# Kernel optimization log

Hardware: AMD Instinct MI355X
Metric: run time of the kernel (lower is better)

## Reference

```python
import jax, jax.numpy as jnp
import numpy as np

B, T, E, A, D, S, N, K = 256, 64, 1024, 32, 1024, 256, 1024, 5
MIN_STD = 0.1


def setup_inputs() -> dict:
    key = jax.random.key(0)
    ks = jax.random.split(key, 16)
    def w(k, shape, scale=0.02):
        return jax.random.normal(k, shape, jnp.float32) * scale
    return dict(
        seq_len=T,
        obs_embed=jax.random.normal(ks[0], (B, T, E), jnp.float32),
        action=jax.random.normal(ks[1], (B, T, A), jnp.float32),
        nonterms=jnp.ones((B, T, 1), jnp.float32),
        init_deter=jax.random.normal(ks[2], (B, D), jnp.float32),
        init_stoch=jax.random.normal(ks[3], (B, S), jnp.float32),
        noise_prior=jax.random.normal(ks[4], (T - 1, B, S), jnp.float32),
        noise_post=jax.random.normal(ks[5], (T - 1, B, S), jnp.float32),
        W_embed=w(ks[6], (S + A, D)), b_embed=jnp.zeros((D,), jnp.float32),
        W_ens=w(ks[7], (K, D, S)), b_ens=jnp.zeros((K, S), jnp.float32),
        W_ih=w(ks[8], (3 * D, D)), W_hh=w(ks[9], (3 * D, D)),
        b_ih=jnp.zeros((3 * D,), jnp.float32), b_hh=jnp.zeros((3 * D,), jnp.float32),
        Wp1=w(ks[10], (D, N)), bp1=jnp.zeros((N,), jnp.float32),
        Wp2=w(ks[11], (N, 2 * S)), bp2=jnp.zeros((2 * S,), jnp.float32),
        Wq1=w(ks[12], (D + E, N)), bq1=jnp.zeros((N,), jnp.float32),
        Wq2=w(ks[13], (N, 2 * S)), bq2=jnp.zeros((2 * S,), jnp.float32),
    )


def _rollout(obs_embed, action, nonterms, init_deter, init_stoch,
             noise_prior, noise_post, W_embed, b_embed, W_ens, b_ens,
             W_ih, W_hh, b_ih, b_hh, Wp1, bp1, Wp2, bp2, Wq1, bq1, Wq2, bq2):
    elu = jax.nn.elu

    def gru(x, h):  # torch.nn.GRUCell math
        gi = x @ W_ih.T + b_ih
        gh = h @ W_hh.T + b_hh
        ir, iz, ig = jnp.split(gi, 3, axis=-1)
        hr, hz, hg = jnp.split(gh, 3, axis=-1)
        r = jax.nn.sigmoid(ir + hr)
        z = jax.nn.sigmoid(iz + hz)
        n = jnp.tanh(ig + r * hg)
        return (1.0 - z) * n + z * h

    def step(carry, xs):
        deter, stoch = carry
        obs_t, act_t, nt, eps_p, eps_q = xs  # nt: [B,1]
        prev_action = act_t * nt
        sa = elu(jnp.concatenate([stoch * nt, prev_action], -1) @ W_embed + b_embed)
        preds = jnp.einsum('bd,kds->kbs', sa, W_ens) + b_ens[:, None, :]  # ensemble heads
        deter_new = gru(sa, deter * nt)
        pm, ps = jnp.split(elu(deter_new @ Wp1 + bp1) @ Wp2 + bp2, 2, -1)
        ps = jax.nn.softplus(ps) + MIN_STD
        prior_stoch = pm + ps * eps_p
        qm, qs = jnp.split(elu(jnp.concatenate([deter_new, obs_t], -1) @ Wq1 + bq1) @ Wq2 + bq2, 2, -1)
        qs = jax.nn.softplus(qs) + MIN_STD
        post_stoch = qm + qs * eps_q
        prior_cat = jnp.concatenate([pm, ps, prior_stoch, deter_new], -1)   # [B, 3S+D]
        post_cat = jnp.concatenate([qm, qs, post_stoch, deter_new], -1)     # [B, 3S+D]
        disag_flat = jnp.transpose(preds, (1, 0, 2)).reshape(preds.shape[1], -1)  # [B, K*S]
        out = jnp.concatenate([prior_cat, post_cat, disag_flat], -1)
        return (deter_new, post_stoch), out

    Tm1 = noise_prior.shape[0]
    xs = (jnp.swapaxes(obs_embed[:, :Tm1], 0, 1),
          jnp.swapaxes(action[:, :Tm1], 0, 1),
          jnp.swapaxes(nonterms[:, :Tm1], 0, 1),
          noise_prior, noise_post)
    _, outs = jax.lax.scan(step, (init_deter, init_stoch), xs)
    return jnp.swapaxes(outs, 0, 1)  # [B, T-1, 2*(3S+D)+K*S]


def reference(seq_len, obs_embed, action, nonterms, init_deter, init_stoch,
              noise_prior, noise_post, W_embed, b_embed, W_ens, b_ens,
              W_ih, W_hh, b_ih, b_hh, Wp1, bp1, Wp2, bp2, Wq1, bq1, Wq2, bq2):
    return _rollout(obs_embed, action, nonterms, init_deter, init_stoch,
                    noise_prior, noise_post, W_embed, b_embed, W_ens, b_ens,
                    W_ih, W_hh, b_ih, b_hh, Wp1, bp1, Wp2, bp2, Wq1, bq1, Wq2, bq2)
```

## Files before the change

kernel.cpp:

```cpp
#include <hip/hip_runtime.h>

typedef float f32x4 __attribute__((ext_vector_type(4)));
typedef __bf16 bf16x8 __attribute__((ext_vector_type(8)));
typedef unsigned short u16;

#define NB 256
#define TT 64
#define TM1 63
#define DD 1024
#define SS 256
#define EE 1024
#define AD 32
#define OUTC 4864
#define OUTT ((size_t)TM1 * OUTC)

__device__ __forceinline__ u16 f2bf(float f) {
    unsigned u = __float_as_uint(f);
    u += 0x7FFFu + ((u >> 16) & 1u);
    return (u16)(u >> 16);
}
__device__ __forceinline__ float sigm(float x) { return 1.f / (1.f + expf(-x)); }
__device__ __forceinline__ float splus(float x) { return x > 15.f ? x : log1pf(expf(x)); }
__device__ __forceinline__ float eluf(float x) { return x > 0.f ? x : (expf(x) - 1.f); }
__device__ __forceinline__ int swz(int row, int cb) { return row * 128 + (cb ^ ((row & 7) << 4)); }

template <class FA, class FE>
__device__ __forceinline__ void gemm_tile(char* As, char* Bs, FA fa,
                                          const u16* __restrict__ Bt, int ldb,
                                          int K, int m0, int n0, FE fe) {
    const int tid = threadIdx.x;
    const int lane = tid & 63;
    const int w = tid >> 6;
    const int wr = (w >> 1) * 32, wc = (w & 1) * 32;
    f32x4 acc00 = {}, acc01 = {}, acc10 = {}, acc11 = {};
    const int r0 = tid >> 3;
    const int ke = (tid & 7) * 8;
    const int cb = (tid & 7) * 16;

    for (int k0 = 0; k0 < K; k0 += 64) {
        uint4 av0 = fa(m0 + r0, k0 + ke);
        uint4 av1 = fa(m0 + r0 + 32, k0 + ke);
        uint4 bv0 = *(const uint4*)(Bt + (size_t)(n0 + r0) * ldb + k0 + ke);
        uint4 bv1 = *(const uint4*)(Bt + (size_t)(n0 + r0 + 32) * ldb + k0 + ke);
        __syncthreads();
        *(uint4*)(As + swz(r0, cb)) = av0;
        *(uint4*)(As + swz(r0 + 32, cb)) = av1;
        *(uint4*)(Bs + swz(r0, cb)) = bv0;
        *(uint4*)(Bs + swz(r0 + 32, cb)) = bv1;
        __syncthreads();
#pragma unroll
        for (int kk = 0; kk < 64; kk += 32) {
            const int fcb = kk * 2 + (lane >> 4) * 16;
            bf16x8 a0 = *(const bf16x8*)(As + swz(wr + (lane & 15), fcb));
            bf16x8 a1 = *(const bf16x8*)(As + swz(wr + 16 + (lane & 15), fcb));
            bf16x8 b0 = *(const bf16x8*)(Bs + swz(wc + (lane & 15), fcb));
            bf16x8 b1 = *(const bf16x8*)(Bs + swz(wc + 16 + (lane & 15), fcb));
            acc00 = __builtin_amdgcn_mfma_f32_16x16x32_bf16(a0, b0, acc00, 0, 0, 0);
            acc01 = __builtin_amdgcn_mfma_f32_16x16x32_bf16(a0, b1, acc01, 0, 0, 0);
            acc10 = __builtin_amdgcn_mfma_f32_16x16x32_bf16(a1, b0, acc10, 0, 0, 0);
            acc11 = __builtin_amdgcn_mfma_f32_16x16x32_bf16(a1, b1, acc11, 0, 0, 0);
        }
    }
    const int er = (lane >> 4) * 4, ec = lane & 15;
#pragma unroll
    for (int r = 0; r < 4; r++) {
        fe(m0 + wr + er + r, n0 + wc + ec, acc00[r]);
        fe(m0 + wr + er + r, n0 + wc + 16 + ec, acc01[r]);
        fe(m0 + wr + 16 + er + r, n0 + wc + ec, acc10[r]);
        fe(m0 + wr + 16 + er + r, n0 + wc + 16 + ec, acc11[r]);
    }
}

__global__ void __launch_bounds__(256) k_cast(const float* __restrict__ in,
                                              u16* __restrict__ out, int n) {
    int i = blockIdx.x * 256 + threadIdx.x;
    if (i < n) out[i] = f2bf(in[i]);
}

__global__ void __launch_bounds__(256) k_transpose(const float* __restrict__ in,
                                                   u16* __restrict__ out,
                                                   int R, int C, int Rpad, int total) {
    int i = blockIdx.x * 256 + threadIdx.x;
    if (i >= total) return;
    int r = i % Rpad;
    int bc = i / Rpad;
    int c = bc % C;
    int bb = bc / C;
    out[i] = (r < R) ? f2bf(in[((size_t)bb * R + r) * C + c]) : (u16)0;
}

__global__ void __launch_bounds__(256) k_prep0(const float* __restrict__ init_deter,
                                               const float* __restrict__ init_stoch,
                                               const float* __restrict__ action,
                                               const float* __restrict__ nonterms,
                                               float* __restrict__ deter,
                                               u16* __restrict__ h_nt,
                                               u16* __restrict__ x_embed) {
    int idx = blockIdx.x * 256 + threadIdx.x;
    int b = idx >> 10, d = idx & 1023;
    float nt0 = nonterms[b * TT + 0];
    float dv = init_deter[idx];
    deter[idx] = dv;
    h_nt[idx] = f2bf(dv * nt0);
    if (d < 256) {
        x_embed[b * 320 + d] = f2bf(init_stoch[b * 256 + d] * nt0);
    } else if (d < 320) {
        int c = d - 256;
        x_embed[b * 320 + d] = (c < AD) ? f2bf(action[(size_t)b * TT * AD + c] * nt0) : (u16)0;
    }
}

__global__ void __launch_bounds__(256) k_gru(const float* __restrict__ gi,
                                             const float* __restrict__ gh,
                                             float* __restrict__ deter,
                                             const float* __restrict__ nonterms, int t,
                                             u16* __restrict__ deter_b,
                                             float* __restrict__ out) {
    int idx = blockIdx.x * 256 + threadIdx.x;
    int b = idx >> 10, d = idx & 1023;
    float nt = nonterms[b * TT + t];
    float h = deter[idx] * nt;
    size_t gb = (size_t)b * 3072;
    float r = sigm(gi[gb + d] + gh[gb + d]);
    float z = sigm(gi[gb + 1024 + d] + gh[gb + 1024 + d]);
    float n = tanhf(gi[gb + 2048 + d] + r * gh[gb + 2048 + d]);
    float dn = (1.f - z) * n + z * h;
    deter[idx] = dn;
    deter_b[idx] = f2bf(dn);
    float* ob = out + (size_t)b * OUTT + (size_t)t * OUTC;
    ob[768 + d] = dn;
    ob[2560 + d] = dn;
}

__global__ void __launch_bounds__(256) k_dist(const float* __restrict__ pout,
                                              const float* __restrict__ qout,
                                              const float* __restrict__ noise_p,
                                              const float* __restrict__ noise_q, int t,
                                              const float* __restrict__ deter,
                                              const float* __restrict__ action,
                                              const float* __restrict__ nonterms,
                                              float* __restrict__ out,
                                              u16* __restrict__ x_embed,
                                              u16* __restrict__ h_nt) {
    int idx = blockIdx.x * 256 + threadIdx.x;
    int b = idx >> 10, d = idx & 1023;
    float ntn = nonterms[b * TT + (t + 1)];
    h_nt[idx] = f2bf(deter[idx] * ntn);
    float* ob = out + (size_t)b * OUTT + (size_t)t * OUTC;
    if (d < 256) {
        int s = d;
        float pm = pout[b * 512 + s];
        float ps = splus(pout[b * 512 + 256 + s]) + 0.1f;
        float ep = noise_p[(size_t)t * (NB * SS) + b * SS + s];
        float pst = pm + ps * ep;
        ob[s] = pm;
        ob[256 + s] = ps;
        ob[512 + s] = pst;
        float qm = qout[b * 512 + s];
        float qs = splus(qout[b * 512 + 256 + s]) + 0.1f;
        float eq = noise_q[(size_t)t * (NB * SS) + b * SS + s];
        float qst = qm + qs * eq;
        ob[1792 + s] = qm;
        ob[2048 + s] = qs;
        ob[2304 + s] = qst;
        x_embed[b * 320 + s] = f2bf(qst * ntn);
    } else if (d < 320) {
        int c = d - 256;
        u16 v = 0;
        if (c < AD) v = f2bf(action[(size_t)b * TT * AD + (size_t)(t + 1) * AD + c] * ntn);
        x_embed[b * 320 + 256 + c] = v;
    }
}

__global__ void __launch_bounds__(256) k_gemm_sa(const u16* __restrict__ xe,
                                                 const u16* __restrict__ Wt,
                                                 const float* __restrict__ bias,
                                                 u16* __restrict__ sa) {
    __shared__ char As[8192];
    __shared__ char Bs[8192];
    int m0 = blockIdx.y * 64, n0 = blockIdx.x * 64;
    auto fa = [&](int r, int k) { return *(const uint4*)(xe + r * 320 + k); };
    auto fe = [&](int r, int n, float v) {
        v = eluf(v + bias[n]);
        sa[r * 1024 + n] = f2bf(v);
    };
    gemm_tile(As, Bs, fa, Wt, 320, 320, m0, n0, fe);
}

__global__ void __launch_bounds__(256) k_gemm_big(const u16* __restrict__ sa,
                                                  const u16* __restrict__ hnt,
                                                  const u16* __restrict__ Wih,
                                                  const u16* __restrict__ Whh,
                                                  const u16* __restrict__ Wens,
                                                  const float* __restrict__ bih,
                                                  const float* __restrict__ bhh,
                                                  const float* __restrict__ bens,
                                                  float* __restrict__ gi,
                                                  float* __restrict__ gh,
                                                  float* __restrict__ dout, int t) {
    __shared__ char As[8192];
    __shared__ char Bs[8192];
    int z = blockIdx.z;
    int m0 = blockIdx.y * 64, n0 = blockIdx.x * 64;
    if (z == 2 && n0 >= 1280) return;
    const u16* Ap = (z == 1) ? hnt : sa;
    auto fa = [&](int r, int k) { return *(const uint4*)(Ap + r * 1024 + k); };
    if (z == 0) {
        auto fe = [&](int r, int n, float v) { gi[(size_t)r * 3072 + n] = v + bih[n]; };
        gemm_tile(As, Bs, fa, Wih, 1024, 1024, m0, n0, fe);
    } else if (z == 1) {
        auto fe = [&](int r, int n, float v) { gh[(size_t)r * 3072 + n] = v + bhh[n]; };
        gemm_tile(As, Bs, fa, Whh, 1024, 1024, m0, n0, fe);
    } else {
        float* op = dout + (size_t)t * OUTC + 3584;
        auto fe = [&](int r, int n, float v) { op[(size_t)r * OUTT + n] = v + bens[n]; };
        gemm_tile(As, Bs, fa, Wens, 1024, 1024, m0, n0, fe);
    }
}

__global__ void __launch_bounds__(256) k_gemm_hpq(const u16* __restrict__ dtb,
                                                  const float* __restrict__ obs,
                                                  const u16* __restrict__ Wp1t,
                                                  const u16* __restrict__ Wq1t,
                                                  const float* __restrict__ bp1,
                                                  const float* __restrict__ bq1,
                                                  u16* __restrict__ hp,
                                                  u16* __restrict__ hq, int t) {
    __shared__ char As[8192];
    __shared__ char Bs[8192];
    int z = blockIdx.z;
    int m0 = blockIdx.y * 64, n0 = blockIdx.x * 64;
    if (z == 0) {
        auto fa = [&](int r, int k) { return *(const uint4*)(dtb + r * 1024 + k); };
        auto fe = [&](int r, int n, float v) {
            v = eluf(v + bp1[n]);
            hp[r * 1024 + n] = f2bf(v);
        };
        gemm_tile(As, Bs, fa, Wp1t, 1024, 1024, m0, n0, fe);
    } else {
        auto fa = [&](int r, int k) {
            if (k < 1024) return *(const uint4*)(dtb + r * 1024 + k);
            const float* q = obs + (size_t)r * (TT * EE) + (size_t)t * EE + (k - 1024);
            float4 f0 = *(const float4*)q, f1 = *(const float4*)(q + 4);
            union { u16 u[8]; uint4 v; } x;
            x.u[0] = f2bf(f0.x); x.u[1] = f2bf(f0.y); x.u[2] = f2bf(f0.z); x.u[3] = f2bf(f0.w);
            x.u[4] = f2bf(f1.x); x.u[5] = f2bf(f1.y); x.u[6] = f2bf(f1.z); x.u[7] = f2bf(f1.w);
            return x.v;
        };
        auto fe = [&](int r, int n, float v) {
            v = eluf(v + bq1[n]);
            hq[r * 1024 + n] = f2bf(v);
        };
        gemm_tile(As, Bs, fa, Wq1t, 2048, 2048, m0, n0, fe);
    }
}

__global__ void __launch_bounds__(256) k_gemm_pq(const u16* __restrict__ hp,
                                                 const u16* __restrict__ hq,
                                                 const u16* __restrict__ Wp2t,
                                                 const u16* __restrict__ Wq2t,
                                                 const float* __restrict__ bp2,
                                                 const float* __restrict__ bq2,
                                                 float* __restrict__ pout,
                                                 float* __restrict__ qout) {
    __shared__ char As[8192];
    __shared__ char Bs[8192];
    int z = blockIdx.z;
    int m0 = blockIdx.y * 64, n0 = blockIdx.x * 64;
    const u16* Ap = z ? hq : hp;
    const u16* Bp = z ? Wq2t : Wp2t;
    const float* bb = z ? bq2 : bp2;
    float* op = z ? qout : pout;
    auto fa = [&](int r, int k) { return *(const uint4*)(Ap + r * 1024 + k); };
    auto fe = [&](int r, int n, float v) { op[r * 512 + n] = v + bb[n]; };
    gemm_tile(As, Bs, fa, Bp, 1024, 1024, m0, n0, fe);
}

extern "C" void kernel_launch(void* const* d_in, const int* in_sizes, int n_in,
                              void* d_out, int out_size, void* d_ws, size_t ws_size,
                              hipStream_t stream) {
    const float* obs = (const float*)d_in[1];
    const float* action = (const float*)d_in[2];
    const float* nonterms = (const float*)d_in[3];
    const float* init_deter = (const float*)d_in[4];
    const float* init_stoch = (const float*)d_in[5];
    const float* noise_p = (const float*)d_in[6];
    const float* noise_q = (const float*)d_in[7];
    const float* W_embed = (const float*)d_in[8];
    const float* b_embed = (const float*)d_in[9];
    const float* W_ens = (const float*)d_in[10];
    const float* b_ens = (const float*)d_in[11];
    const float* W_ih = (const float*)d_in[12];
    const float* W_hh = (const float*)d_in[13];
    const float* b_ih = (const float*)d_in[14];
    const float* b_hh = (const float*)d_in[15];
    const float* Wp1 = (const float*)d_in[16];
    const float* bp1 = (const float*)d_in[17];
    const float* Wp2 = (const float*)d_in[18];
    const float* bp2 = (const float*)d_in[19];
    const float* Wq1 = (const float*)d_in[20];
    const float* bq1 = (const float*)d_in[21];
    const float* Wq2 = (const float*)d_in[22];
    const float* bq2 = (const float*)d_in[23];
    float* out = (float*)d_out;

    char* ws = (char*)d_ws;
    size_t off = 0;
    auto alloc = [&](size_t bytes) {
        void* p = ws + off;
        off += (bytes + 255) & ~(size_t)255;
        return p;
    };
    u16* Wembed_t = (u16*)alloc(1024 * 320 * 2);
    u16* Wih_b = (u16*)alloc(3072 * 1024 * 2);
    u16* Whh_b = (u16*)alloc(3072 * 1024 * 2);
    u16* Wens_t = (u16*)alloc(1280 * 1024 * 2);
    u16* Wp1_t = (u16*)alloc(1024 * 1024 * 2);
    u16* Wp2_t = (u16*)alloc(512 * 1024 * 2);
    u16* Wq1_t = (u16*)alloc((size_t)1024 * 2048 * 2);
    u16* Wq2_t = (u16*)alloc(512 * 1024 * 2);
    u16* x_embed = (u16*)alloc(256 * 320 * 2);
    u16* h_nt = (u16*)alloc(256 * 1024 * 2);
    u16* sa = (u16*)alloc(256 * 1024 * 2);
    float* deter = (float*)alloc(256 * 1024 * 4);
    u16* deter_b = (u16*)alloc(256 * 1024 * 2);
    float* gi = (float*)alloc((size_t)256 * 3072 * 4);
    float* gh = (float*)alloc((size_t)256 * 3072 * 4);
    u16* hp = (u16*)alloc(256 * 1024 * 2);
    u16* hq = (u16*)alloc(256 * 1024 * 2);
    float* pout = (float*)alloc(256 * 512 * 4);
    float* qout = (float*)alloc(256 * 512 * 4);
    (void)ws_size;

    {
        int tot = 1024 * 320;
        k_transpose<<<(tot + 255) / 256, 256, 0, stream>>>(W_embed, Wembed_t, 288, 1024, 320, tot);
        int nc = 3072 * 1024;
        k_cast<<<(nc + 255) / 256, 256, 0, stream>>>(W_ih, Wih_b, nc);
        k_cast<<<(nc + 255) / 256, 256, 0, stream>>>(W_hh, Whh_b, nc);
        tot = 5 * 256 * 1024;
        k_transpose<<<(tot + 255) / 256, 256, 0, stream>>>(W_ens, Wens_t, 1024, 256, 1024, tot);
        tot = 1024 * 1024;
        k_transpose<<<(tot + 255) / 256, 256, 0, stream>>>(Wp1, Wp1_t, 1024, 1024, 1024, tot);
        tot = 512 * 1024;
        k_transpose<<<(tot + 255) / 256, 256, 0, stream>>>(Wp2, Wp2_t, 1024, 512, 1024, tot);
        tot = 1024 * 2048;
        k_transpose<<<(tot + 255) / 256, 256, 0, stream>>>(Wq1, Wq1_t, 2048, 1024, 2048, tot);
        tot = 512 * 1024;
        k_transpose<<<(tot + 255) / 256, 256, 0, stream>>>(Wq2, Wq2_t, 1024, 512, 1024, tot);
    }

    k_prep0<<<1024, 256, 0, stream>>>(init_deter, init_stoch, action, nonterms,
                                      deter, h_nt, x_embed);

    for (int t = 0; t < TM1; t++) {
        k_gemm_sa<<<dim3(16, 4), 256, 0, stream>>>(x_embed, Wembed_t, b_embed, sa);
        k_gemm_big<<<dim3(48, 4, 3), 256, 0, stream>>>(sa, h_nt, Wih_b, Whh_b, Wens_t,
                                                       b_ih, b_hh, b_ens, gi, gh, out, t);
        k_gru<<<1024, 256, 0, stream>>>(gi, gh, deter, nonterms, t, deter_b, out);
        k_gemm_hpq<<<dim3(16, 4, 2), 256, 0, stream>>>(deter_b, obs, Wp1_t, Wq1_t,
                                                       bp1, bq1, hp, hq, t);
        k_gemm_pq<<<dim3(8, 4, 2), 256, 0, stream>>>(hp, hq, Wp2_t, Wq2_t, bp2, bq2,
                                                     pout, qout);
        k_dist<<<1024, 256, 0, stream>>>(pout, qout, noise_p, noise_q, t, deter,
                                         action, nonterms, out, x_embed, h_nt);
    }
}
```

Measured before the change: 4.888 ms.

## Fuse distribution head epilogue into second projection GEMM and drop k_dist

A dual-B-tile GEMM computes the mean and std columns for the same rows in one block, so softplus, noise sampling, output writes and the next x_embed update can happen in the GEMM epilogue. The h_nt and action parts of x_embed move into the GRU kernel, which removes the separate k_dist launch and the pout/qout round trip each step. The cost is that the fused GEMM grid halves to 32 blocks, each doing twice the MFMA work with more shared memory and registers.

```diff
diff --git a/kernel.cpp b/kernel.cpp
--- a/kernel.cpp
+++ b/kernel.cpp
@@ -71,6 +71,64 @@
     }
 }
 
+template <class FA, class FE>
+__device__ __forceinline__ void gemm_tile2(char* As, char* Bs0, char* Bs1, FA fa,
+                                           const u16* __restrict__ Bt, int ldb,
+                                           int K, int m0, int n0, int nstr, FE fe) {
+    const int tid = threadIdx.x;
+    const int lane = tid & 63;
+    const int w = tid >> 6;
+    const int wr = (w >> 1) * 32, wc = (w & 1) * 32;
+    f32x4 a00 = {}, a01 = {}, a10 = {}, a11 = {};
+    f32x4 c00 = {}, c01 = {}, c10 = {}, c11 = {};
+    const int r0 = tid >> 3;
+    const int ke = (tid & 7) * 8;
+    const int cb = (tid & 7) * 16;
+
+    for (int k0 = 0; k0 < K; k0 += 64) {
+        uint4 av0 = fa(m0 + r0, k0 + ke);
+        uint4 av1 = fa(m0 + r0 + 32, k0 + ke);
+        uint4 b0v0 = *(const uint4*)(Bt + (size_t)(n0 + r0) * ldb + k0 + ke);
+        uint4 b0v1 = *(const uint4*)(Bt + (size_t)(n0 + r0 + 32) * ldb + k0 + ke);
+        uint4 b1v0 = *(const uint4*)(Bt + (size_t)(n0 + nstr + r0) * ldb + k0 + ke);
+        uint4 b1v1 = *(const uint4*)(Bt + (size_t)(n0 + nstr + r0 + 32) * ldb + k0 + ke);
+        __syncthreads();
+        *(uint4*)(As + swz(r0, cb)) = av0;
+        *(uint4*)(As + swz(r0 + 32, cb)) = av1;
+        *(uint4*)(Bs0 + swz(r0, cb)) = b0v0;
+        *(uint4*)(Bs0 + swz(r0 + 32, cb)) = b0v1;
+        *(uint4*)(Bs1 + swz(r0, cb)) = b1v0;
+        *(uint4*)(Bs1 + swz(r0 + 32, cb)) = b1v1;
+        __syncthreads();
+#pragma unroll
+        for (int kk = 0; kk < 64; kk += 32) {
+            const int fcb = kk * 2 + (lane >> 4) * 16;
+            bf16x8 a0 = *(const bf16x8*)(As + swz(wr + (lane & 15), fcb));
+            bf16x8 a1 = *(const bf16x8*)(As + swz(wr + 16 + (lane & 15), fcb));
+            bf16x8 b0 = *(const bf16x8*)(Bs0 + swz(wc + (lane & 15), fcb));
+            bf16x8 b1 = *(const bf16x8*)(Bs0 + swz(wc + 16 + (lane & 15), fcb));
+            bf16x8 d0 = *(const bf16x8*)(Bs1 + swz(wc + (lane & 15), fcb));
+            bf16x8 d1 = *(const bf16x8*)(Bs1 + swz(wc + 16 + (lane & 15), fcb));
+            a00 = __builtin_amdgcn_mfma_f32_16x16x32_bf16(a0, b0, a00, 0, 0, 0);
+            a01 = __builtin_amdgcn_mfma_f32_16x16x32_bf16(a0, b1, a01, 0, 0, 0);
+            a10 = __builtin_amdgcn_mfma_f32_16x16x32_bf16(a1, b0, a10, 0, 0, 0);
+            a11 = __builtin_amdgcn_mfma_f32_16x16x32_bf16(a1, b1, a11, 0, 0, 0);
+            c00 = __builtin_amdgcn_mfma_f32_16x16x32_bf16(a0, d0, c00, 0, 0, 0);
+            c01 = __builtin_amdgcn_mfma_f32_16x16x32_bf16(a0, d1, c01, 0, 0, 0);
+            c10 = __builtin_amdgcn_mfma_f32_16x16x32_bf16(a1, d0, c10, 0, 0, 0);
+            c11 = __builtin_amdgcn_mfma_f32_16x16x32_bf16(a1, d1, c11, 0, 0, 0);
+        }
+    }
+    const int er = (lane >> 4) * 4, ec = lane & 15;
+#pragma unroll
+    for (int r = 0; r < 4; r++) {
+        fe(m0 + wr + er + r, n0 + wc + ec, a00[r], c00[r]);
+        fe(m0 + wr + er + r, n0 + wc + 16 + ec, a01[r], c01[r]);
+        fe(m0 + wr + 16 + er + r, n0 + wc + ec, a10[r], c10[r]);
+        fe(m0 + wr + 16 + er + r, n0 + wc + 16 + ec, a11[r], c11[r]);
+    }
+}
+
 __global__ void __launch_bounds__(256) k_cast(const float* __restrict__ in,
                                               u16* __restrict__ out, int n) {
     int i = blockIdx.x * 256 + threadIdx.x;
@@ -113,8 +171,11 @@
 __global__ void __launch_bounds__(256) k_gru(const float* __restrict__ gi,
                                              const float* __restrict__ gh,
                                              float* __restrict__ deter,
-                                             const float* __restrict__ nonterms, int t,
+                                             const float* __restrict__ nonterms,
+                                             const float* __restrict__ action, int t,
                                              u16* __restrict__ deter_b,
+                                             u16* __restrict__ h_nt,
+                                             u16* __restrict__ x_embed,
                                              float* __restrict__ out) {
     int idx = blockIdx.x * 256 + threadIdx.x;
     int b = idx >> 10, d = idx & 1023;
@@ -127,45 +188,13 @@
     float dn = (1.f - z) * n + z * h;
     deter[idx] = dn;
     deter_b[idx] = f2bf(dn);
+    float ntn = nonterms[b * TT + t + 1];
+    h_nt[idx] = f2bf(dn * ntn);
     float* ob = out + (size_t)b * OUTT + (size_t)t * OUTC;
     ob[768 + d] = dn;
     ob[2560 + d] = dn;
-}
-
-__global__ void __launch_bounds__(256) k_dist(const float* __restrict__ pout,
-                                              const float* __restrict__ qout,
-                                              const float* __restrict__ noise_p,
-                                              const float* __restrict__ noise_q, int t,
-                                              const float* __restrict__ deter,
-                                              const float* __restrict__ action,
-                                              const float* __restrict__ nonterms,
-                                              float* __restrict__ out,
-                                              u16* __restrict__ x_embed,
-                                              u16* __restrict__ h_nt) {
-    int idx = blockIdx.x * 256 + threadIdx.x;
-    int b = idx >> 10, d = idx & 1023;
-    float ntn = nonterms[b * TT + (t + 1)];
-    h_nt[idx] = f2bf(deter[idx] * ntn);
-    float* ob = out + (size_t)b * OUTT + (size_t)t * OUTC;
-    if (d < 256) {
-        int s = d;
-        float pm = pout[b * 512 + s];
-        float ps = splus(pout[b * 512 + 256 + s]) + 0.1f;
-        float ep = noise_p[(size_t)t * (NB * SS) + b * SS + s];
-        float pst = pm + ps * ep;
-        ob[s] = pm;
-        ob[256 + s] = ps;
-        ob[512 + s] = pst;
-        float qm = qout[b * 512 + s];
-        float qs = splus(qout[b * 512 + 256 + s]) + 0.1f;
-        float eq = noise_q[(size_t)t * (NB * SS) + b * SS + s];
-        float qst = qm + qs * eq;
-        ob[1792 + s] = qm;
-        ob[2048 + s] = qs;
-        ob[2304 + s] = qst;
-        x_embed[b * 320 + s] = f2bf(qst * ntn);
-    } else if (d < 320) {
-        int c = d - 256;
+    if (d < 64) {
+        int c = d;
         u16 v = 0;
         if (c < AD) v = f2bf(action[(size_t)b * TT * AD + (size_t)(t + 1) * AD + c] * ntn);
         x_embed[b * 320 + 256 + c] = v;
@@ -255,25 +284,43 @@
     }
 }
 
-__global__ void __launch_bounds__(256) k_gemm_pq(const u16* __restrict__ hp,
+__global__ void __launch_bounds__(256) k_pq_dist(const u16* __restrict__ hp,
                                                  const u16* __restrict__ hq,
                                                  const u16* __restrict__ Wp2t,
                                                  const u16* __restrict__ Wq2t,
                                                  const float* __restrict__ bp2,
                                                  const float* __restrict__ bq2,
-                                                 float* __restrict__ pout,
-                                                 float* __restrict__ qout) {
+                                                 const float* __restrict__ noise_p,
+                                                 const float* __restrict__ noise_q,
+                                                 const float* __restrict__ nonterms,
+                                                 float* __restrict__ out,
+                                                 u16* __restrict__ x_embed, int t) {
     __shared__ char As[8192];
-    __shared__ char Bs[8192];
+    __shared__ char Bs0[8192];
+    __shared__ char Bs1[8192];
     int z = blockIdx.z;
     int m0 = blockIdx.y * 64, n0 = blockIdx.x * 64;
     const u16* Ap = z ? hq : hp;
     const u16* Bp = z ? Wq2t : Wp2t;
-    const float* bb = z ? bq2 : bp2;
-    float* op = z ? qout : pout;
+    const float* b2 = z ? bq2 : bp2;
+    const float* noise = z ? noise_q : noise_p;
+    const int obase = z ? 1792 : 0;
     auto fa = [&](int r, int k) { return *(const uint4*)(Ap + r * 1024 + k); };
-    auto fe = [&](int r, int n, float v) { op[r * 512 + n] = v + bb[n]; };
-    gemm_tile(As, Bs, fa, Bp, 1024, 1024, m0, n0, fe);
+    auto fe = [&](int r, int s, float mv, float sv) {
+        float m = mv + b2[s];
+        float sd = splus(sv + b2[s + 256]) + 0.1f;
+        float eps = noise[(size_t)t * (NB * SS) + r * SS + s];
+        float st = m + sd * eps;
+        float* obp = out + (size_t)r * OUTT + (size_t)t * OUTC + obase;
+        obp[s] = m;
+        obp[256 + s] = sd;
+        obp[512 + s] = st;
+        if (z) {
+            float ntn = nonterms[r * TT + t + 1];
+            x_embed[r * 320 + s] = f2bf(st * ntn);
+        }
+    };
+    gemm_tile2(As, Bs0, Bs1, fa, Bp, 1024, 1024, m0, n0, 256, fe);
 }
 
 extern "C" void kernel_launch(void* const* d_in, const int* in_sizes, int n_in,
@@ -328,8 +375,6 @@
     float* gh = (float*)alloc((size_t)256 * 3072 * 4);
     u16* hp = (u16*)alloc(256 * 1024 * 2);
     u16* hq = (u16*)alloc(256 * 1024 * 2);
-    float* pout = (float*)alloc(256 * 512 * 4);
-    float* qout = (float*)alloc(256 * 512 * 4);
     (void)ws_size;
 
     {
@@ -357,12 +402,12 @@
         k_gemm_sa<<<dim3(16, 4), 256, 0, stream>>>(x_embed, Wembed_t, b_embed, sa);
         k_gemm_big<<<dim3(48, 4, 3), 256, 0, stream>>>(sa, h_nt, Wih_b, Whh_b, Wens_t,
                                                        b_ih, b_hh, b_ens, gi, gh, out, t);
-        k_gru<<<1024, 256, 0, stream>>>(gi, gh, deter, nonterms, t, deter_b, out);
+        k_gru<<<1024, 256, 0, stream>>>(gi, gh, deter, nonterms, action, t,
+                                        deter_b, h_nt, x_embed, out);
         k_gemm_hpq<<<dim3(16, 4, 2), 256, 0, stream>>>(deter_b, obs, Wp1_t, Wq1_t,
                                                        bp1, bq1, hp, hq, t);
-        k_gemm_pq<<<dim3(8, 4, 2), 256, 0, stream>>>(hp, hq, Wp2_t, Wq2_t, bp2, bq2,
-                                                     pout, qout);
-        k_dist<<<1024, 256, 0, stream>>>(pout, qout, noise_p, noise_q, t, deter,
-                                         action, nonterms, out, x_embed, h_nt);
-    }
-}
+        k_pq_dist<<<dim3(4, 4, 2), 256, 0, stream>>>(hp, hq, Wp2_t, Wq2_t, bp2, bq2,
+                                                     noise_p, noise_q, nonterms,
+                                                     out, x_embed, t);
+    }
+}
```

Result: slower. 5.701 ms (+16.6%).
